# Optimization experiments

Measured on AMD Instinct MI355X. Metric: run time of the kernel, lower is better.

## Reference

```python
import jax, jax.numpy as jnp
import numpy as np

C = 1.0          # Poincare ball curvature
EPS = 1e-15
N, K, X, H = 16384, 16, 256, 256

def _artanh(x):
    return jnp.arctanh(jnp.clip(x, -1 + 1e-5, 1 - 1e-5))

def _norm(x):
    return jnp.sqrt(jnp.clip(jnp.sum(x * x, -1, keepdims=True), EPS))

def _proj(x):
    n = _norm(x)
    maxn = (1.0 - 1e-5) / np.sqrt(C)
    return jnp.where(n > maxn, x / n * maxn, x)

def mobius_add(x, y):
    x2 = jnp.sum(x * x, -1, keepdims=True)
    y2 = jnp.sum(y * y, -1, keepdims=True)
    xy = jnp.sum(x * y, -1, keepdims=True)
    num = (1 + 2 * C * xy + C * y2) * x + (1 - C * x2) * y
    den = 1 + 2 * C * xy + C * C * x2 * y2
    return _proj(num / jnp.clip(den, EPS))

def expmap0(u):
    sc = np.sqrt(C); un = _norm(u)
    return _proj(jnp.tanh(sc * un) * u / (sc * un))

def logmap0(x):
    sc = np.sqrt(C); xn = _norm(x)
    return _artanh(sc * xn) * x / (sc * xn)

def mobius_matvec(M, x):
    sc = np.sqrt(C); xn = _norm(x)
    mx = x @ M.T
    mxn = _norm(mx)
    return _proj(jnp.tanh(mxn / xn * _artanh(sc * xn)) * mx / (mxn * sc))

def mobius_pointwise_mul(w, x):
    # geoopt order: norm taken on x, product w*x
    sc = np.sqrt(C); xn = _norm(x)
    wx = w * x
    wxn = _norm(wx)
    return _proj(jnp.tanh(wxn / xn * _artanh(sc * xn)) * wx / (wxn * sc))

def mobius_scalar_mul(r, x):
    sc = np.sqrt(C); xn = _norm(x)
    return _proj(jnp.tanh(r * _artanh(sc * xn)) * x / (xn * sc))

def weighted_midpoint(x, axis):
    # geoopt weighted_midpoint with uniform weights, reducedim=[axis]
    lam = 2.0 / jnp.clip(1 - C * jnp.sum(x * x, -1, keepdims=True), EPS)
    num = jnp.sum(lam * x, axis=axis)
    den = jnp.sum(lam - 1.0, axis=axis)
    den = jnp.where(jnp.abs(den) < 1e-10, 1e-10, den)
    return mobius_scalar_mul(0.5, num / den)

def hyper_attn(h_, x_, g_t):
    # tangent-space scaled dot-product attention with Hawkes-decay bias
    q = logmap0(x_)                                   # [N,h]
    k = logmap0(h_)                                   # [N,K,h]
    logits = jnp.einsum('nkh,nh->nk', k, q) / np.sqrt(k.shape[-1]) + g_t
    return jax.nn.softmax(logits, axis=-1)            # [N,K]

def setup_inputs() -> dict:
    key = jax.random.key(0)
    ks = jax.random.split(key, 12)
    stdv = 1.0 / np.sqrt(H)
    u = lambda k, s: jax.random.uniform(k, s, jnp.float32, -stdv, stdv)
    return dict(
        x=0.5 * jax.random.normal(ks[0], (N, X), jnp.float32),
        h1=expmap0(0.05 * jax.random.normal(ks[1], (N, H), jnp.float32)),
        c1=expmap0(0.05 * jax.random.normal(ks[2], (N, H), jnp.float32)),
        del_t=10.0 * jax.random.uniform(ks[3], (N,), jnp.float32),
        edges=jax.random.randint(ks[4], (N, K), 0, N),
        W_iou=u(ks[5], (3 * H, X)), U_iou=u(ks[6], (3 * H, H)), b_iou=jnp.zeros((1, 3 * H)),
        U_f=u(ks[7], (H, H)),
        W_q=u(ks[8], (H, X)), b_q=jnp.zeros((1, H)),
        W_k=u(ks[9], (H, H)), b_k=jnp.zeros((1, H)),
        W_c=u(ks[10], (H, H)), b_c=jnp.zeros((1, H)),
        b_haw=jnp.array([1e-6], jnp.float32), a_haw=jnp.array([0.02], jnp.float32),
        haw_1=jnp.array([1.0], jnp.float32), haw_2=jnp.array([1.0], jnp.float32),
    )

def reference(x, h1, c1, del_t, edges, W_iou, U_iou, b_iou, U_f, W_q, b_q, W_k, b_k, W_c, b_c, b_haw, a_haw, haw_1, haw_2):
    Hm = h1[edges]                     # mailbox h1  [N,K,h]
    Cm = c1[edges]                     # mailbox c1  [N,K,h]
    dt = del_t[edges]                  # mailbox del_t [N,K]
    g_t = b_haw * jnp.exp(-a_haw * dt)                       # [N,K]
    x_ball = expmap0(x)
    # --- reduce_func ---
    x_q = mobius_add(mobius_matvec(W_q, x_ball), b_q)         # [N,h]
    h_k = mobius_add(mobius_matvec(W_k, Hm), b_k)             # [N,K,h]
    scores = hyper_attn(h_k, x_q, g_t)                        # [N,K]
    h_scaled = mobius_pointwise_mul(scores[..., None], Hm)
    decay = jnp.exp(-haw_2 * dt / 60.0)[..., None]
    h_max = mobius_pointwise_mul(jax.nn.relu(h_scaled), decay)
    h_hawkes = mobius_add(h_scaled, haw_1 * h_max)
    h_tild = weighted_midpoint(h_hawkes, axis=1)              # [N,h]
    c_sk = expmap0(jnp.tanh(logmap0(mobius_add(mobius_matvec(W_c, Cm), b_c))))
    c_sk_hat = mobius_pointwise_mul(c_sk, g_t[..., None])
    c_k_tilde = mobius_add(mobius_add(-c_sk, Cm), c_sk_hat)
    f = jax.nn.sigmoid(logmap0(mobius_matvec(U_f, Hm)))
    c_red = weighted_midpoint(mobius_pointwise_mul(f, c_k_tilde), axis=1)
    iou0 = mobius_matvec(W_iou, x_ball)                       # [N,3h]
    iou1 = mobius_add(iou0, mobius_matvec(U_iou, h_tild))
    # --- apply_node_func ---
    iou = mobius_add(iou1, b_iou)
    i, o, u2 = jnp.split(iou, 3, axis=1)
    i = jax.nn.sigmoid(logmap0(i))
    o = jax.nn.sigmoid(logmap0(o))
    u2 = jnp.tanh(logmap0(u2))
    c_new = mobius_add(mobius_pointwise_mul(i, u2), c_red)
    h_new = mobius_pointwise_mul(o, jnp.tanh(logmap0(c_new)))
    return h_new, c_new
```

## Files before the change

### kernel.cpp

```cpp
#include <hip/hip_runtime.h>
#include <math.h>

#define NN 16384
#define D  256
#define NB (NN*D)
#define EPSR 1e-15f
#define SQEPS 3.1622776601683794e-8f
#define MXN 0.99999f

typedef unsigned short u16;
typedef __bf16 bf16x8 __attribute__((ext_vector_type(8)));
typedef float f32x4 __attribute__((ext_vector_type(4)));
typedef unsigned short u16x8 __attribute__((ext_vector_type(8)));
typedef unsigned short u16x4 __attribute__((ext_vector_type(4)));

__device__ __forceinline__ float fexp(float x){ return __builtin_amdgcn_exp2f(x * 1.4426950408889634f); }
__device__ __forceinline__ float flog(float x){ return __builtin_amdgcn_logf(x) * 0.6931471805599453f; }
__device__ __forceinline__ float frcp(float x){ return __builtin_amdgcn_rcpf(x); }
__device__ __forceinline__ float fsqrt(float x){ return __builtin_amdgcn_sqrtf(x); }
__device__ __forceinline__ float ftanh(float x){
  float xc = fminf(fmaxf(x, -15.f), 15.f);
  float t = fexp(2.f * xc);
  return (t - 1.f) * frcp(t + 1.f);
}
__device__ __forceinline__ float at_c(float x){
  float xc = fminf(fmaxf(x, -1.f + 1e-5f), 1.f - 1e-5f);
  return 0.5f * flog((1.f + xc) * frcp(1.f - xc));
}
__device__ __forceinline__ float fsig(float x){ return frcp(1.f + fexp(-x)); }

__device__ __forceinline__ float b2f(u16 u){
  unsigned int x = ((unsigned int)u) << 16;
  return __builtin_bit_cast(float, x);
}
__device__ __forceinline__ u16 f2b(float f){
  unsigned int u = __builtin_bit_cast(unsigned int, f);
  return (u16)((u + 0x7fffu + ((u >> 16) & 1u)) >> 16);
}
__device__ __forceinline__ float wred(float v){
#pragma unroll
  for (int m = 32; m; m >>= 1) v += __shfl_xor(v, m);
  return v;
}
__device__ __forceinline__ float sig_proj(float npre, float* nrm){
  float n = fmaxf(npre, SQEPS);
  float s = (n > MXN) ? (MXN * frcp(n)) : 1.f;
  *nrm = fminf(n, MXN);
  return s;
}
__device__ __forceinline__ void ld4(const u16* p, float v[4]){
  u16x4 t = *(const u16x4*)p;
#pragma unroll
  for (int r = 0; r < 4; r++) v[r] = b2f(t[r]);
}
__device__ __forceinline__ void ld4f(const float* p, float v[4]){
  f32x4 t = *(const f32x4*)p;
#pragma unroll
  for (int r = 0; r < 4; r++) v[r] = t[r];
}

__global__ void __launch_bounds__(256) k_wcvt(
    const float* __restrict__ Wq, const float* __restrict__ Wiou,
    const float* __restrict__ Wk, const float* __restrict__ Uf,
    const float* __restrict__ Wc, const float* __restrict__ Uiou,
    u16* __restrict__ dst)
{
  size_t base = ((size_t)blockIdx.x * 256 + threadIdx.x) * 4;
  const float* src; size_t off;
  if      (base <  65536){ src = Wq;   off = base; }
  else if (base < 262144){ src = Wiou; off = base - 65536; }
  else if (base < 327680){ src = Wk;   off = base - 262144; }
  else if (base < 393216){ src = Uf;   off = base - 327680; }
  else if (base < 458752){ src = Wc;   off = base - 393216; }
  else                   { src = Uiou; off = base - 458752; }
  f32x4 v = *(const f32x4*)(src + off);
  u16x4 o;
#pragma unroll
  for (int r = 0; r < 4; r++) o[r] = f2b(v[r]);
  *(u16x4*)(dst + base) = o;
}

__global__ void __launch_bounds__(256) k_prep(const float* __restrict__ x,
    const float* __restrict__ h1, const float* __restrict__ c1,
    u16* __restrict__ xbb, u16* __restrict__ cb, u16* __restrict__ pack,
    float* __restrict__ scal)
{
  int w = threadIdx.x >> 6, lane = threadIdx.x & 63;
  int n = blockIdx.x * 4 + w;
  int base = n * D + lane * 4;
  float xv[4], hv[4], cv[4];
  ld4f(x + base, xv); ld4f(h1 + base, hv); ld4f(c1 + base, cv);
  float un2 = 0, hn2 = 0, prn2 = 0, cn2 = 0;
#pragma unroll
  for (int r = 0; r < 4; r++){
    un2 += xv[r]*xv[r]; hn2 += hv[r]*hv[r];
    float rr = fmaxf(hv[r], 0.f); prn2 += rr*rr;
    cn2 += cv[r]*cv[r];
  }
  un2 = wred(un2); hn2 = wred(hn2); prn2 = wred(prn2); cn2 = wred(cn2);
  float un = fsqrt(fmaxf(un2, EPSR));
  float t  = ftanh(un);
  float sc = t * frcp(un);
  float nx = fsqrt(fmaxf(sc*sc*un2, EPSR));
  float s  = (nx > MXN) ? (MXN * frcp(nx)) : 1.f;
  u16x4 ox, oh, oc;
#pragma unroll
  for (int r = 0; r < 4; r++){ ox[r] = f2b(s*sc*xv[r]); oh[r] = f2b(hv[r]); oc[r] = f2b(cv[r]); }
  *(u16x4*)(xbb + base) = ox;
  *(u16x4*)(cb + base) = oc;
  *(u16x4*)(pack + (size_t)n*768 + lane*4) = oh;
  if (lane == 0){
    float* sp = scal + (size_t)n * 16;
    sp[0] = fminf(nx, MXN);
    sp[1] = hn2; sp[2] = prn2; sp[3] = cn2;
    float hn = fsqrt(fmaxf(hn2, EPSR));
    sp[9] = at_c(hn); sp[10] = hn;
  }
}

#define TM 128
#define TN 128
#define TK 32
#define LDP 40
__global__ void __launch_bounds__(256) gemm_bt(const u16* __restrict__ A, int lda,
    const u16* __restrict__ B, u16* __restrict__ C, int K, int Nout)
{
  __shared__ u16 As[TM*LDP];
  __shared__ u16 Bs[TN*LDP];
  int t = threadIdx.x;
  int m0 = blockIdx.x * TM, n0 = blockIdx.y * TN;
  int w = t >> 6, lane = t & 63;
  int wr = w >> 1, wc = w & 1;
  int q = lane >> 4, l16 = lane & 15;
  f32x4 acc[4][4];
#pragma unroll
  for (int i = 0; i < 4; i++)
#pragma unroll
    for (int j = 0; j < 4; j++) acc[i][j] = (f32x4){0.f,0.f,0.f,0.f};
  for (int k0 = 0; k0 < K; k0 += TK){
    __syncthreads();
#pragma unroll
    for (int c = t; c < 512; c += 256){
      int row = c >> 2, ko = (c & 3) * 8;
      *(u16x8*)(As + row*LDP + ko) = *(const u16x8*)(A + (size_t)(m0+row)*lda + k0 + ko);
      *(u16x8*)(Bs + row*LDP + ko) = *(const u16x8*)(B + (size_t)(n0+row)*K + k0 + ko);
    }
    __syncthreads();
    bf16x8 af[4], bfr[4];
#pragma unroll
    for (int rb = 0; rb < 4; rb++)
      af[rb] = *(const bf16x8*)(As + (wr*64 + rb*16 + l16)*LDP + q*8);
#pragma unroll
    for (int cb2 = 0; cb2 < 4; cb2++)
      bfr[cb2] = *(const bf16x8*)(Bs + (wc*64 + cb2*16 + l16)*LDP + q*8);
#pragma unroll
    for (int rb = 0; rb < 4; rb++)
#pragma unroll
      for (int cb2 = 0; cb2 < 4; cb2++)
        acc[rb][cb2] = __builtin_amdgcn_mfma_f32_16x16x32_bf16(af[rb], bfr[cb2], acc[rb][cb2], 0, 0, 0);
  }
#pragma unroll
  for (int rb = 0; rb < 4; rb++)
#pragma unroll
    for (int cb2 = 0; cb2 < 4; cb2++)
#pragma unroll
      for (int r = 0; r < 4; r++){
        int m  = m0 + wr*64 + rb*16 + q*4 + r;
        int nn = n0 + wc*64 + cb2*16 + l16;
        C[(size_t)m*Nout + nn] = f2b(acc[rb][cb2][r]);
      }
}

__device__ __forceinline__ float mm_madd(const float mv[4], const float bv[4], float xn, float z[4]){
  float mn2 = 0.f;
#pragma unroll
  for (int r = 0; r < 4; r++) mn2 += mv[r]*mv[r];
  mn2 = wred(mn2);
  float mnc = fsqrt(fmaxf(mn2, EPSR));
  float imnc = frcp(mnc);
  float t = ftanh(mnc * frcp(xn) * at_c(xn));
  float npre = t * fsqrt(mn2) * imnc;
  float nf; float sg = sig_proj(npre, &nf);
  float cx = sg * t * imnc;
  float x2 = (sg*npre)*(sg*npre);
  float y2 = 0.f, xy = 0.f;
#pragma unroll
  for (int r = 0; r < 4; r++){ y2 += bv[r]*bv[r]; xy += cx*mv[r]*bv[r]; }
  y2 = wred(y2); xy = wred(xy);
  float A = 1.f + 2.f*xy + y2, Bc = 1.f - x2;
  float idn = frcp(fmaxf(1.f + 2.f*xy + x2*y2, EPSR));
  float zn2 = (A*A*x2 + 2.f*A*Bc*xy + Bc*Bc*y2) * idn * idn;
  float zn = fsqrt(fmaxf(zn2, EPSR));
  float sz = (zn > MXN) ? (MXN * frcp(zn)) : 1.f;
  float ca = sz * A * idn * cx, cb = sz * Bc * idn;
#pragma unroll
  for (int r = 0; r < 4; r++) z[r] = ca*mv[r] + cb*bv[r];
  return fminf(zn, MXN);
}

__global__ void __launch_bounds__(256) k_post(
    const u16* __restrict__ mqiou, const u16* __restrict__ mkf,
    const u16* __restrict__ mc,
    const float* __restrict__ c1,
    const float* __restrict__ bq, const float* __restrict__ bk, const float* __restrict__ bc,
    u16* __restrict__ qv, u16* __restrict__ kv,
    u16* __restrict__ pack,
    float* __restrict__ scal)
{
  int w = threadIdx.x >> 6, lane = threadIdx.x & 63;
  int n = blockIdx.x * 4 + w;
  int base = n * D + lane * 4, lb = lane * 4;
  float* sp = scal + (size_t)n * 16;
  float xbn = sp[0], hn2 = sp[1], cn2 = sp[3];
  float hnc = fsqrt(fmaxf(hn2, EPSR));
  float cnc = fsqrt(fmaxf(cn2, EPSR));
  float mv[4], bv[4], z[4];
  u16x4 o;
  ld4(mqiou + (size_t)n*1024 + lb, mv); ld4f(bq + lb, bv);
  float znf = mm_madd(mv, bv, xbn, z);
  float cl = at_c(znf) * frcp(znf);
#pragma unroll
  for (int r = 0; r < 4; r++) o[r] = f2b(cl * z[r]);
  *(u16x4*)(qv + base) = o;
  ld4(mkf + (size_t)n*512 + lb, mv); ld4f(bk + lb, bv);
  znf = mm_madd(mv, bv, hnc, z);
  cl = at_c(znf) * frcp(znf);
#pragma unroll
  for (int r = 0; r < 4; r++) o[r] = f2b(cl * z[r]);
  *(u16x4*)(kv + base) = o;
  float fv[4];
  {
    ld4(mkf + (size_t)n*512 + 256 + lb, mv);
    float mn2 = 0.f;
#pragma unroll
    for (int r = 0; r < 4; r++) mn2 += mv[r]*mv[r];
    mn2 = wred(mn2);
    float mnc = fsqrt(fmaxf(mn2, EPSR));
    float imnc = frcp(mnc);
    float t = ftanh(mnc * frcp(hnc) * at_c(hnc));
    float npre = t * fsqrt(mn2) * imnc;
    float nf; float sg = sig_proj(npre, &nf);
    float cx = sg * t * imnc;
    float lcf = at_c(nf) * frcp(nf);
#pragma unroll
    for (int r = 0; r < 4; r++) fv[r] = fsig(lcf * cx * mv[r]);
  }
  float csk[4];
  {
    ld4(mc + base, mv); ld4f(bc + lb, bv);
    float zn = mm_madd(mv, bv, cnc, z);
    float lc = at_c(zn) * frcp(zn);
    float th[4]; float thn2 = 0.f;
#pragma unroll
    for (int r = 0; r < 4; r++){ th[r] = ftanh(lc * z[r]); thn2 += th[r]*th[r]; }
    thn2 = wred(thn2);
    float thn = fsqrt(fmaxf(thn2, EPSR));
    float te = ftanh(thn);
    float se = te * frcp(thn);
    float npe = fsqrt(fmaxf(se*se*thn2, EPSR));
    float sge = (npe > MXN) ? (MXN * frcp(npe)) : 1.f;
#pragma unroll
    for (int r = 0; r < 4; r++) csk[r] = sge * se * th[r];
  }
  float c1v[4]; ld4f(c1 + base, c1v);
  float csn2 = 0, pcc = 0, pfss = 0, pfsm = 0, pfmm = 0;
#pragma unroll
  for (int r = 0; r < 4; r++){
    float f2 = fv[r]*fv[r];
    csn2 += csk[r]*csk[r];
    pcc  += csk[r]*c1v[r];
    pfss += f2*csk[r]*csk[r];
    pfsm += f2*csk[r]*c1v[r];
    pfmm += f2*c1v[r]*c1v[r];
  }
  csn2 = wred(csn2); pcc = wred(pcc); pfss = wred(pfss); pfsm = wred(pfsm); pfmm = wred(pfmm);
  u16x4 oa, ob;
#pragma unroll
  for (int r = 0; r < 4; r++){ oa[r] = f2b(fv[r]*csk[r]); ob[r] = f2b(fv[r]*c1v[r]); }
  *(u16x4*)(pack + (size_t)n*768 + 256 + lb) = oa;
  *(u16x4*)(pack + (size_t)n*768 + 512 + lb) = ob;
  if (lane == 0){
    sp[4] = csn2; sp[5] = pcc; sp[6] = pfss; sp[7] = pfsm; sp[8] = pfmm;
  }
}

__global__ void __launch_bounds__(256) k_logit(
    const int* __restrict__ edges, const float* __restrict__ del_t,
    const u16* __restrict__ qv, const u16* __restrict__ kvec,
    const float* __restrict__ pbh, const float* __restrict__ pah,
    float* __restrict__ logit)
{
  int w = threadIdx.x >> 6, lane = threadIdx.x & 63;
  int n = blockIdx.x * 4 + w;
  float bh = pbh[0], ah = pah[0];
  float qf[4]; ld4(qv + n*D + lane*4, qf);
  for (int k = 0; k < 16; k++){
    int j = edges[n*16 + k];
    float dt = del_t[j];
    u16x4 kt = *(const u16x4*)(kvec + (size_t)j*D + lane*4);
    float d = 0.f;
#pragma unroll
    for (int r = 0; r < 4; r++) d += qf[r] * b2f(kt[r]);
    d = wred(d);
    if (lane == 0) logit[n*16 + k] = d * 0.0625f + bh * fexp(-ah * dt);
  }
}

__global__ void __launch_bounds__(256) k_coef(
    const int* __restrict__ edges, const float* __restrict__ del_t,
    const float* __restrict__ logit, const float* __restrict__ scal,
    const float* __restrict__ pbh, const float* __restrict__ pah,
    const float* __restrict__ ph1, const float* __restrict__ ph2,
    float* __restrict__ coef)
{
  int e = blockIdx.x * 256 + threadIdx.x;
  int n = e >> 4;
  int j = edges[e];
  float dt = del_t[j];
  float bh = pbh[0], ah = pah[0], hw1 = ph1[0], hw2 = ph2[0];
  const float* ln = logit + n*16;
  float mxl = -1e30f;
#pragma unroll
  for (int k = 0; k < 16; k++) mxl = fmaxf(mxl, ln[k]);
  float sume = 0.f;
#pragma unroll
  for (int k = 0; k < 16; k++) sume += fexp(ln[k] - mxl);
  float sk = fexp(ln[e & 15] - mxl) * frcp(sume);
  const float* sp2 = scal + (size_t)j * 16;
  float hn2 = sp2[1], prn2 = sp2[2], cn2 = sp2[3], csn2 = sp2[4], pcc = sp2[5],
        pfss = sp2[6], pfsm = sp2[7], pfmm = sp2[8], athn = sp2[9], hn = sp2[10];
  float g = bh * fexp(-ah * dt);
  float decay = fexp(-hw2 * dt * (1.f/60.f));
  float wxn1 = fsqrt(fmaxf(sk*sk*hn2, EPSR));
  float iwxn1 = frcp(wxn1);
  float t1 = ftanh(wxn1 * frcp(hn) * athn);
  float npre1 = t1 * sk * fsqrt(hn2) * iwxn1;
  float nn1 = fmaxf(npre1, SQEPS); float sg1 = (nn1 > MXN) ? MXN*frcp(nn1) : 1.f;
  float a_h = sg1 * t1 * sk * iwxn1;
  float rn2 = a_h*a_h*prn2;
  float xnd  = fsqrt(fmaxf(decay*decay, EPSR));
  float wxn2 = fsqrt(fmaxf(decay*decay*rn2, EPSR));
  float iwxn2 = frcp(wxn2);
  float t2 = ftanh(wxn2 * frcp(xnd) * at_c(xnd));
  float npre2 = t2 * decay * fsqrt(rn2) * iwxn2;
  float nn2 = fmaxf(npre2, SQEPS); float sg2 = (nn2 > MXN) ? MXN*frcp(nn2) : 1.f;
  float b_h = sg2 * t2 * decay * a_h * iwxn2;
  float bh1 = hw1 * b_h;
  float x2 = a_h*a_h*hn2;
  float y2 = bh1*bh1*prn2;
  float xy = a_h*bh1*prn2;
  float A = 1.f + 2.f*xy + y2, B = 1.f - x2;
  float idn = frcp(fmaxf(1.f + 2.f*xy + x2*y2, EPSR));
  float nh2 = (A*A*x2 + 2.f*A*B*xy + B*B*y2) * idn * idn;
  float nh = fsqrt(fmaxf(nh2, EPSR)); float sg3 = (nh > MXN) ? MXN*frcp(nh) : 1.f;
  float p  = sg3 * A * a_h * idn;
  float rr = sg3 * B * bh1 * idn;
  float hhn2 = sg3*sg3*nh2;
  float lam = 2.f * frcp(fmaxf(1.f - hhn2, EPSR));
  float xng  = fsqrt(fmaxf(g*g, EPSR));
  float wxn3 = fsqrt(fmaxf(g*g*csn2, EPSR));
  float iwxn3 = frcp(wxn3);
  float t3 = ftanh(wxn3 * frcp(xng) * at_c(xng));
  float npre3 = t3 * g * fsqrt(csn2) * iwxn3;
  float nn3 = fmaxf(npre3, SQEPS); float sgc = (nn3 > MXN) ? MXN*frcp(nn3) : 1.f;
  float gam = sgc * t3 * g * iwxn3;
  float A1 = 1.f - 2.f*pcc + cn2, B1 = 1.f - csn2;
  float iden1 = frcp(fmaxf(1.f - 2.f*pcc + csn2*cn2, EPSR));
  float al = -A1*iden1, be = B1*iden1;
  float n1sq = al*al*csn2 + 2.f*al*be*pcc + be*be*cn2;
  float n1 = fsqrt(fmaxf(n1sq, EPSR)); float s1 = (n1 > MXN) ? MXN*frcp(n1) : 1.f;
  al *= s1; be *= s1;
  float z1n2 = s1*s1*n1sq;
  float y2c = gam*gam*csn2;
  float xyc = gam*(al*csn2 + be*pcc);
  float A2 = 1.f + 2.f*xyc + y2c, B2 = 1.f - z1n2;
  float iden2 = frcp(fmaxf(1.f + 2.f*xyc + z1n2*y2c, EPSR));
  float u1 = (A2*al + B2*gam)*iden2, u2 = A2*be*iden2;
  float n2sq = u1*u1*csn2 + 2.f*u1*u2*pcc + u2*u2*cn2;
  float n2 = fsqrt(fmaxf(n2sq, EPSR)); float s2 = (n2 > MXN) ? MXN*frcp(n2) : 1.f;
  u1 *= s2; u2 *= s2;
  float xnc = fminf(n2, MXN);
  float wx2 = u1*u1*pfss + 2.f*u1*u2*pfsm + u2*u2*pfmm;
  float wxn4 = fsqrt(fmaxf(wx2, EPSR));
  float iwxn4 = frcp(wxn4);
  float t4 = ftanh(wxn4 * frcp(xnc) * at_c(xnc));
  float npre4 = t4 * fsqrt(wx2) * iwxn4;
  float nn4 = fmaxf(npre4, SQEPS); float s4 = (nn4 > MXN) ? MXN*frcp(nn4) : 1.f;
  float v1 = s4*t4*u1*iwxn4, v2 = s4*t4*u2*iwxn4;
  float rsn2 = (s4*npre4)*(s4*npre4);
  float lam2 = 2.f * frcp(fmaxf(1.f - rsn2, EPSR));
  float* cf = coef + (size_t)e * 6;
  cf[0] = lam; cf[1] = lam*p; cf[2] = lam*rr;
  cf[3] = lam2; cf[4] = lam2*v1; cf[5] = lam2*v2;
}

__global__ void __launch_bounds__(256) k_acc(
    const int* __restrict__ edges, const u16* __restrict__ pack,
    const float* __restrict__ coef,
    u16* __restrict__ ht, u16* __restrict__ cred, float* __restrict__ htn_arr)
{
  int w = threadIdx.x >> 6, lane = threadIdx.x & 63;
  int n = blockIdx.x * 4 + w;
  float numh[4] = {0,0,0,0}, numc[4] = {0,0,0,0};
  float denh = 0.f, denc = 0.f;
#pragma unroll 4
  for (int k = 0; k < 16; k++){
    int e = n*16 + k;
    int j = edges[e];
    const float* cf = coef + (size_t)e * 6;
    float lam = cf[0], lamp = cf[1], lamr = cf[2];
    float lam2 = cf[3], lv1 = cf[4], lv2 = cf[5];
    denh += lam - 1.f; denc += lam2 - 1.f;
    const u16* pr = pack + (size_t)j*768 + lane*4;
    u16x4 hx4 = *(const u16x4*)(pr);
    u16x4 fs4 = *(const u16x4*)(pr + 256);
    u16x4 fm4 = *(const u16x4*)(pr + 512);
#pragma unroll
    for (int r = 0; r < 4; r++){
      float hxr = b2f(hx4[r]);
      numh[r] += lamp*hxr + lamr*fmaxf(hxr, 0.f);
      numc[r] += lv1*b2f(fs4[r]) + lv2*b2f(fm4[r]);
    }
  }
  if (fabsf(denh) < 1e-10f) denh = 1e-10f;
  if (fabsf(denc) < 1e-10f) denc = 1e-10f;
  float idh = frcp(denh), idc = frcp(denc);
  float vh[4], vc[4]; float vn2h = 0.f, vn2c = 0.f;
#pragma unroll
  for (int r = 0; r < 4; r++){
    vh[r] = numh[r]*idh; vn2h += vh[r]*vh[r];
    vc[r] = numc[r]*idc; vn2c += vc[r]*vc[r];
  }
  vn2h = wred(vn2h); vn2c = wred(vn2c);
  float vnh = fsqrt(fmaxf(vn2h, EPSR));
  float tth = ftanh(0.5f * at_c(vnh));
  float nph = tth * fsqrt(vn2h) * frcp(vnh);
  float nfh; float sh = sig_proj(nph, &nfh);
  float chh = sh * tth * frcp(vnh);
  u16x4 ho;
#pragma unroll
  for (int r = 0; r < 4; r++) ho[r] = f2b(chh * vh[r]);
  *(u16x4*)(ht + (size_t)n*D + lane*4) = ho;
  if (lane == 0) htn_arr[n] = nfh;
  float vnc = fsqrt(fmaxf(vn2c, EPSR));
  float ttc = ftanh(0.5f * at_c(vnc));
  float npc = ttc * fsqrt(vn2c) * frcp(vnc);
  float nfc; float scz = sig_proj(npc, &nfc);
  float chc = scz * ttc * frcp(vnc);
  u16x4 co;
#pragma unroll
  for (int r = 0; r < 4; r++) co[r] = f2b(chc * vc[r]);
  *(u16x4*)(cred + (size_t)n*D + lane*4) = co;
}

__global__ void __launch_bounds__(256) k_final(
    const u16* __restrict__ mqiou, const u16* __restrict__ mu,
    const u16* __restrict__ cred, const float* __restrict__ biou,
    const float* __restrict__ scal, const float* __restrict__ htn_arr,
    float* __restrict__ out)
{
  int w = threadIdx.x >> 6, lane = threadIdx.x & 63;
  int n = blockIdx.x * 4 + w;
  float mi[3][4], muv[3][4], bi[3][4];
#pragma unroll
  for (int p = 0; p < 3; p++){
    ld4(mqiou + (size_t)n*1024 + 256 + p*256 + lane*4, mi[p]);
    ld4(mu   + (size_t)n*768 + p*256 + lane*4, muv[p]);
    ld4f(biou + p*256 + lane*4, bi[p]);
  }
  float cr[4]; ld4(cred + (size_t)n*D + lane*4, cr);
  float xbn = scal[(size_t)n*16 + 0];
  float htn = htn_arr[n];
  float mn2 = 0.f, un2 = 0.f, dmu = 0.f;
#pragma unroll
  for (int p = 0; p < 3; p++)
#pragma unroll
    for (int r = 0; r < 4; r++){
      mn2 += mi[p][r]*mi[p][r]; un2 += muv[p][r]*muv[p][r]; dmu += mi[p][r]*muv[p][r];
    }
  mn2 = wred(mn2); un2 = wred(un2); dmu = wred(dmu);
  float mnc = fsqrt(fmaxf(mn2, EPSR));
  float ta = ftanh(mnc * frcp(xbn) * at_c(xbn));
  float npa = ta * fsqrt(mn2) * frcp(mnc);
  float na_; float sa = sig_proj(npa, &na_);
  float ca = sa * ta * frcp(mnc); float x2 = (sa*npa)*(sa*npa);
  float unc = fsqrt(fmaxf(un2, EPSR));
  float tb = ftanh(unc * frcp(htn) * at_c(htn));
  float npb = tb * fsqrt(un2) * frcp(unc);
  float nb_; float sb = sig_proj(npb, &nb_);
  float cb = sb * tb * frcp(unc); float y2 = (sb*npb)*(sb*npb);
  float xy = ca * cb * dmu;
  float A = 1.f + 2.f*xy + y2, B = 1.f - x2;
  float idn = frcp(fmaxf(1.f + 2.f*xy + x2*y2, EPSR));
  float c_mi = A*ca*idn, c_mu = B*cb*idn;
  float n1sq = (A*A*x2 + 2.f*A*B*xy + B*B*y2) * idn * idn;
  float n1 = fsqrt(fmaxf(n1sq, EPSR)); float s1 = (n1 > MXN) ? MXN*frcp(n1) : 1.f;
  c_mi *= s1; c_mu *= s1;
  float iou1n2 = s1*s1*n1sq;
  float io1[3][4]; float bb2 = 0.f, xyb = 0.f;
#pragma unroll
  for (int p = 0; p < 3; p++)
#pragma unroll
    for (int r = 0; r < 4; r++){
      io1[p][r] = c_mi*mi[p][r] + c_mu*muv[p][r];
      bb2 += bi[p][r]*bi[p][r]; xyb += io1[p][r]*bi[p][r];
    }
  bb2 = wred(bb2); xyb = wred(xyb);
  float A2 = 1.f + 2.f*xyb + bb2, B2 = 1.f - iou1n2;
  float iden2 = frcp(fmaxf(1.f + 2.f*xyb + iou1n2*bb2, EPSR));
  float n2sq = (A2*A2*iou1n2 + 2.f*A2*B2*xyb + B2*B2*bb2) * iden2 * iden2;
  float n2c = fsqrt(fmaxf(n2sq, EPSR)); float s2 = (n2c > MXN) ? MXN*frcp(n2c) : 1.f;
  float cA2 = s2*A2*iden2, cB2 = s2*B2*iden2;
  float iou[3][4];
#pragma unroll
  for (int p = 0; p < 3; p++)
#pragma unroll
    for (int r = 0; r < 4; r++) iou[p][r] = cA2*io1[p][r] + cB2*bi[p][r];
  float ni2 = 0.f, no2 = 0.f, nu2 = 0.f;
#pragma unroll
  for (int r = 0; r < 4; r++){ ni2 += iou[0][r]*iou[0][r]; no2 += iou[1][r]*iou[1][r]; nu2 += iou[2][r]*iou[2][r]; }
  ni2 = wred(ni2); no2 = wred(no2); nu2 = wred(nu2);
  float niN = fsqrt(fmaxf(ni2, EPSR)), noN = fsqrt(fmaxf(no2, EPSR)), nuN = fsqrt(fmaxf(nu2, EPSR));
  float ci = at_c(niN)*frcp(niN), co = at_c(noN)*frcp(noN), cu = at_c(nuN)*frcp(nuN);
  float iv[4], ov[4], uv[4];
#pragma unroll
  for (int r = 0; r < 4; r++){
    iv[r] = fsig(ci*iou[0][r]);
    ov[r] = fsig(co*iou[1][r]);
    uv[r] = ftanh(cu*iou[2][r]);
  }
  float xn2 = 0.f, wn2 = 0.f; float wx[4];
#pragma unroll
  for (int r = 0; r < 4; r++){ xn2 += uv[r]*uv[r]; wx[r] = iv[r]*uv[r]; wn2 += wx[r]*wx[r]; }
  xn2 = wred(xn2); wn2 = wred(wn2);
  float xnc = fsqrt(fmaxf(xn2, EPSR)), wnc = fsqrt(fmaxf(wn2, EPSR));
  float t4 = ftanh(wnc * frcp(xnc) * at_c(xnc));
  float np4 = t4 * fsqrt(wn2) * frcp(wnc);
  float n4_; float s4 = sig_proj(np4, &n4_);
  float cpm = s4*t4*frcp(wnc); float pmn2 = (s4*np4)*(s4*np4);
  float y2c = 0.f, xyc = 0.f;
#pragma unroll
  for (int r = 0; r < 4; r++){ y2c += cr[r]*cr[r]; xyc += cpm*wx[r]*cr[r]; }
  y2c = wred(y2c); xyc = wred(xyc);
  float A3 = 1.f + 2.f*xyc + y2c, B3 = 1.f - pmn2;
  float iden3 = frcp(fmaxf(1.f + 2.f*xyc + pmn2*y2c, EPSR));
  float n3sq = (A3*A3*pmn2 + 2.f*A3*B3*xyc + B3*B3*y2c) * iden3 * iden3;
  float n3 = fsqrt(fmaxf(n3sq, EPSR)); float s3 = (n3 > MXN) ? MXN*frcp(n3) : 1.f;
  float cA3 = s3*A3*cpm*iden3, cB3 = s3*B3*iden3;
  float cnw[4]; f32x4 oc;
#pragma unroll
  for (int r = 0; r < 4; r++){ cnw[r] = cA3*wx[r] + cB3*cr[r]; oc[r] = cnw[r]; }
  *(f32x4*)(out + NB + (size_t)n*D + lane*4) = oc;
  float ncn = fminf(n3, MXN);
  float clg = at_c(ncn)*frcp(ncn);
  float th[4]; float xn5 = 0.f, wn5 = 0.f; float wx5[4];
#pragma unroll
  for (int r = 0; r < 4; r++){
    th[r] = ftanh(clg*cnw[r]);
    xn5 += th[r]*th[r]; wx5[r] = ov[r]*th[r]; wn5 += wx5[r]*wx5[r];
  }
  xn5 = wred(xn5); wn5 = wred(wn5);
  float xn5c = fsqrt(fmaxf(xn5, EPSR)), wn5c = fsqrt(fmaxf(wn5, EPSR));
  float t5 = ftanh(wn5c * frcp(xn5c) * at_c(xn5c));
  float np5 = t5 * fsqrt(wn5) * frcp(wn5c);
  float n5_; float s5 = sig_proj(np5, &n5_);
  float ch = s5*t5*frcp(wn5c);
  f32x4 oh;
#pragma unroll
  for (int r = 0; r < 4; r++) oh[r] = ch * wx5[r];
  *(f32x4*)(out + (size_t)n*D + lane*4) = oh;
}

extern "C" void kernel_launch(void* const* d_in, const int* in_sizes, int n_in,
                              void* d_out, int out_size, void* d_ws, size_t ws_size,
                              hipStream_t stream)
{
  (void)in_sizes; (void)n_in; (void)out_size; (void)ws_size;
  const float* x     = (const float*)d_in[0];
  const float* h1    = (const float*)d_in[1];
  const float* c1    = (const float*)d_in[2];
  const float* del_t = (const float*)d_in[3];
  const int*   edges = (const int*)d_in[4];
  const float* W_iou = (const float*)d_in[5];
  const float* U_iou = (const float*)d_in[6];
  const float* b_iou = (const float*)d_in[7];
  const float* U_f   = (const float*)d_in[8];
  const float* W_q   = (const float*)d_in[9];
  const float* b_q   = (const float*)d_in[10];
  const float* W_k   = (const float*)d_in[11];
  const float* b_k   = (const float*)d_in[12];
  const float* W_c   = (const float*)d_in[13];
  const float* b_c   = (const float*)d_in[14];
  const float* b_haw = (const float*)d_in[15];
  const float* a_haw = (const float*)d_in[16];
  const float* haw1  = (const float*)d_in[17];
  const float* haw2  = (const float*)d_in[18];

  u16* wb    = (u16*)d_ws;
  u16* xbb   = wb + 655360;
  u16* cb    = xbb + NB;
  u16* pack  = cb + NB;
  u16* mqiou = pack + (size_t)NN*768;
  u16* mkf   = mqiou + 4*(size_t)NB;
  u16* mc    = mkf + 2*(size_t)NB;
  u16* qv    = mc + NB;
  u16* kvec  = qv + NB;
  float* scal    = (float*)(kvec + NB);
  float* logit   = scal + (size_t)NN*16;
  float* htn_arr = logit + (size_t)NN*16;
  u16* ht   = xbb;
  u16* cred = qv;
  float* coef = (float*)kvec;
  u16* mu   = mkf;

  k_wcvt<<<640, 256, 0, stream>>>(W_q, W_iou, W_k, U_f, W_c, U_iou, wb);
  k_prep<<<NN/4, 256, 0, stream>>>(x, h1, c1, xbb, cb, pack, scal);
  gemm_bt<<<dim3(NN/128, 8), 256, 0, stream>>>(xbb, 256, wb,          mqiou, 256, 1024);
  gemm_bt<<<dim3(NN/128, 4), 256, 0, stream>>>(pack, 768, wb+262144,  mkf,   256, 512);
  gemm_bt<<<dim3(NN/128, 2), 256, 0, stream>>>(cb,  256, wb+393216,   mc,    256, 256);
  k_post<<<NN/4, 256, 0, stream>>>(mqiou, mkf, mc, c1, b_q, b_k, b_c, qv, kvec, pack, scal);
  k_logit<<<NN/4, 256, 0, stream>>>(edges, del_t, qv, kvec, b_haw, a_haw, logit);
  k_coef<<<NN*16/256, 256, 0, stream>>>(edges, del_t, logit, scal, b_haw, a_haw, haw1, haw2, coef);
  k_acc<<<NN/4, 256, 0, stream>>>(edges, pack, coef, ht, cred, htn_arr);
  gemm_bt<<<dim3(NN/128, 6), 256, 0, stream>>>(ht, 256, wb+458752, mu, 256, 768);
  k_final<<<NN/4, 256, 0, stream>>>(mqiou, mu, cred, b_iou, scal, htn_arr, (float*)d_out);
}
```

Before: 338.3 us.

## Fuse logit and coefficient kernels; split edge accumulation across two waves per node

Merges k_logit and k_coef into one kernel. Per-node logits, neighbor ids and dt values go through shared memory instead of a global logit buffer, which removes one launch and a global round trip. k_acc now assigns two waves per node, each summing 8 of the 16 edges, and combines the partial sums through LDS. This doubles the wave count for the gather-bound accumulation to expose more memory parallelism. The coefficient buffer moves to its own workspace region instead of aliasing kvec. The cost is that only 16 of 64 lanes stay active for the coefficient math, and there is an extra block-level barrier.

```diff
diff --git a/kernel.cpp b/kernel.cpp
--- a/kernel.cpp
+++ b/kernel.cpp
@@ -284,16 +284,22 @@
   }
 }
 
-__global__ void __launch_bounds__(256) k_logit(
+__global__ void __launch_bounds__(256) k_lgc(
     const int* __restrict__ edges, const float* __restrict__ del_t,
     const u16* __restrict__ qv, const u16* __restrict__ kvec,
+    const float* __restrict__ scal,
     const float* __restrict__ pbh, const float* __restrict__ pah,
-    float* __restrict__ logit)
-{
+    const float* __restrict__ ph1, const float* __restrict__ ph2,
+    float* __restrict__ coef)
+{
+  __shared__ int   s_j[4][16];
+  __shared__ float s_dt[4][16];
+  __shared__ float s_lg[4][16];
   int w = threadIdx.x >> 6, lane = threadIdx.x & 63;
   int n = blockIdx.x * 4 + w;
-  float bh = pbh[0], ah = pah[0];
+  float bh = pbh[0], ah = pah[0], hw1 = ph1[0], hw2 = ph2[0];
   float qf[4]; ld4(qv + n*D + lane*4, qf);
+#pragma unroll
   for (int k = 0; k < 16; k++){
     int j = edges[n*16 + k];
     float dt = del_t[j];
@@ -302,30 +308,21 @@
 #pragma unroll
     for (int r = 0; r < 4; r++) d += qf[r] * b2f(kt[r]);
     d = wred(d);
-    if (lane == 0) logit[n*16 + k] = d * 0.0625f + bh * fexp(-ah * dt);
-  }
-}
-
-__global__ void __launch_bounds__(256) k_coef(
-    const int* __restrict__ edges, const float* __restrict__ del_t,
-    const float* __restrict__ logit, const float* __restrict__ scal,
-    const float* __restrict__ pbh, const float* __restrict__ pah,
-    const float* __restrict__ ph1, const float* __restrict__ ph2,
-    float* __restrict__ coef)
-{
-  int e = blockIdx.x * 256 + threadIdx.x;
-  int n = e >> 4;
-  int j = edges[e];
-  float dt = del_t[j];
-  float bh = pbh[0], ah = pah[0], hw1 = ph1[0], hw2 = ph2[0];
-  const float* ln = logit + n*16;
+    if (lane == 0){ s_j[w][k] = j; s_dt[w][k] = dt; s_lg[w][k] = d * 0.0625f + bh * fexp(-ah * dt); }
+  }
+  __syncthreads();
+  if (lane >= 16) return;
+  int e = n*16 + lane;
+  int j = s_j[w][lane];
+  float dt = s_dt[w][lane];
+  const float* ln = s_lg[w];
   float mxl = -1e30f;
 #pragma unroll
   for (int k = 0; k < 16; k++) mxl = fmaxf(mxl, ln[k]);
   float sume = 0.f;
 #pragma unroll
   for (int k = 0; k < 16; k++) sume += fexp(ln[k] - mxl);
-  float sk = fexp(ln[e & 15] - mxl) * frcp(sume);
+  float sk = fexp(ln[lane] - mxl) * frcp(sume);
   const float* sp2 = scal + (size_t)j * 16;
   float hn2 = sp2[1], prn2 = sp2[2], cn2 = sp2[3], csn2 = sp2[4], pcc = sp2[5],
         pfss = sp2[6], pfsm = sp2[7], pfmm = sp2[8], athn = sp2[9], hn = sp2[10];
@@ -399,12 +396,17 @@
     const float* __restrict__ coef,
     u16* __restrict__ ht, u16* __restrict__ cred, float* __restrict__ htn_arr)
 {
+  __shared__ f32x4 s_nh[2][64];
+  __shared__ f32x4 s_nc[2][64];
+  __shared__ float s_d[2][2];
   int w = threadIdx.x >> 6, lane = threadIdx.x & 63;
-  int n = blockIdx.x * 4 + w;
+  int nb = w >> 1, half = w & 1;
+  int n = blockIdx.x * 2 + nb;
   float numh[4] = {0,0,0,0}, numc[4] = {0,0,0,0};
   float denh = 0.f, denc = 0.f;
-#pragma unroll 4
-  for (int k = 0; k < 16; k++){
+#pragma unroll
+  for (int kk = 0; kk < 8; kk++){
+    int k = half*8 + kk;
     int e = n*16 + k;
     int j = edges[e];
     const float* cf = coef + (size_t)e * 6;
@@ -421,6 +423,21 @@
       numh[r] += lamp*hxr + lamr*fmaxf(hxr, 0.f);
       numc[r] += lv1*b2f(fs4[r]) + lv2*b2f(fm4[r]);
     }
+  }
+  if (half == 1){
+    f32x4 a, b;
+#pragma unroll
+    for (int r = 0; r < 4; r++){ a[r] = numh[r]; b[r] = numc[r]; }
+    s_nh[nb][lane] = a; s_nc[nb][lane] = b;
+    if (lane == 0){ s_d[nb][0] = denh; s_d[nb][1] = denc; }
+  }
+  __syncthreads();
+  if (half == 1) return;
+  {
+    f32x4 a = s_nh[nb][lane], b = s_nc[nb][lane];
+#pragma unroll
+    for (int r = 0; r < 4; r++){ numh[r] += a[r]; numc[r] += b[r]; }
+    denh += s_d[nb][0]; denc += s_d[nb][1];
   }
   if (fabsf(denh) < 1e-10f) denh = 1e-10f;
   if (fabsf(denc) < 1e-10f) denc = 1e-10f;
@@ -606,11 +623,10 @@
   u16* qv    = mc + NB;
   u16* kvec  = qv + NB;
   float* scal    = (float*)(kvec + NB);
-  float* logit   = scal + (size_t)NN*16;
-  float* htn_arr = logit + (size_t)NN*16;
+  float* coefbuf = scal + (size_t)NN*16;
+  float* htn_arr = coefbuf + (size_t)NN*96;
   u16* ht   = xbb;
   u16* cred = qv;
-  float* coef = (float*)kvec;
   u16* mu   = mkf;
 
   k_wcvt<<<640, 256, 0, stream>>>(W_q, W_iou, W_k, U_f, W_c, U_iou, wb);
@@ -619,9 +635,8 @@
   gemm_bt<<<dim3(NN/128, 4), 256, 0, stream>>>(pack, 768, wb+262144,  mkf,   256, 512);
   gemm_bt<<<dim3(NN/128, 2), 256, 0, stream>>>(cb,  256, wb+393216,   mc,    256, 256);
   k_post<<<NN/4, 256, 0, stream>>>(mqiou, mkf, mc, c1, b_q, b_k, b_c, qv, kvec, pack, scal);
-  k_logit<<<NN/4, 256, 0, stream>>>(edges, del_t, qv, kvec, b_haw, a_haw, logit);
-  k_coef<<<NN*16/256, 256, 0, stream>>>(edges, del_t, logit, scal, b_haw, a_haw, haw1, haw2, coef);
-  k_acc<<<NN/4, 256, 0, stream>>>(edges, pack, coef, ht, cred, htn_arr);
+  k_lgc<<<NN/4, 256, 0, stream>>>(edges, del_t, qv, kvec, scal, b_haw, a_haw, haw1, haw2, coefbuf);
+  k_acc<<<NN/2, 256, 0, stream>>>(edges, pack, coefbuf, ht, cred, htn_arr);
   gemm_bt<<<dim3(NN/128, 6), 256, 0, stream>>>(ht, 256, wb+458752, mu, 256, 768);
   k_final<<<NN/4, 256, 0, stream>>>(mqiou, mu, cred, b_iou, scal, htn_arr, (float*)d_out);
 }
```

New measurement: 334.6 us. About the same (-1.1%).
